# Performance work log

Measured on AMD Instinct MI355X. Metric: run time of the kernel, lower is better.

## Reference

```python
import jax, jax.numpy as jnp
import numpy as np

VOCAB, E, H, L, B, T, S, V = 32000, 512, 1024, 2, 64, 64, 128, 1024
LSTM_IN = 2 * E  # input_feed=True -> cat(embed, prev_output)


def setup_inputs() -> dict:
    key = jax.random.key(0)
    ks = jax.random.split(key, 12)
    s = lambda *d: 1.0 / np.sqrt(d[-1])
    return {
        "tgt_batch": jax.random.randint(ks[0], (T, B), 0, VOCAB),
        "h_encoder": jax.random.normal(ks[1], (B, S, V), jnp.float32),
        "emb": jax.random.normal(ks[2], (VOCAB, E), jnp.float32) * 0.02,
        "output_init": jnp.zeros((B, E), jnp.float32),
        "hidden_init": jnp.zeros((L, B, H), jnp.float32),
        "W_ih": jax.random.uniform(ks[3], (L, 4 * H, LSTM_IN), jnp.float32, -s(H), s(H)),
        "W_hh": jax.random.uniform(ks[4], (L, 4 * H, H), jnp.float32, -s(H), s(H)),
        "b_ih": jax.random.uniform(ks[5], (L, 4 * H), jnp.float32, -s(H), s(H)),
        "b_hh": jax.random.uniform(ks[6], (L, 4 * H), jnp.float32, -s(H), s(H)),
        "W1": jax.random.uniform(ks[7], (V, H), jnp.float32, -s(H), s(H)),   # query_size->values_size
        "b1": jnp.zeros((V,), jnp.float32),
        "W2": jax.random.uniform(ks[8], (E, H + V), jnp.float32, -s(H + V), s(H + V)),
        "b2": jnp.zeros((E,), jnp.float32),
    }


def reference(tgt_batch, h_encoder, emb, output_init, hidden_init,
              W_ih, W_hh, b_ih, b_hh, W1, b1, W2, b2):
    x_seq = emb[tgt_batch]  # [T, B, E]

    def lstm_cell(x, h, c):  # x:[B,2E], h/c:[L,B,H]
        hs, cs, inp = [], [], x
        for l in range(L):
            gates = inp @ W_ih[l].T + b_ih[l] + h[l] @ W_hh[l].T + b_hh[l]
            i, f, g, o = jnp.split(gates, 4, axis=-1)  # torch gate order i,f,g,o
            c_new = jax.nn.sigmoid(f) * c[l] + jax.nn.sigmoid(i) * jnp.tanh(g)
            h_new = jax.nn.sigmoid(o) * jnp.tanh(c_new)
            hs.append(h_new); cs.append(c_new); inp = h_new
        return jnp.stack(hs), jnp.stack(cs), inp

    def global_attn(query):  # query:[B,H]
        q = query @ W1.T + b1                              # [B,V]
        scores = jnp.einsum('bv,bsv->bs', q, h_encoder)    # [B,S]
        a = jax.nn.softmax(scores, axis=-1)
        attended = jnp.einsum('bs,bsv->bv', a, h_encoder)  # [B,V]
        return jnp.tanh(jnp.concatenate([attended, query], axis=-1) @ W2.T + b2)

    def step(carry, x):
        h, c, out = carry
        inp = jnp.concatenate([x, out], axis=-1)  # input feed
        h, c, top = lstm_cell(inp, h, c)
        o = global_attn(top)  # dropout is identity in eval mode
        return (h, c, o), o

    c0 = jnp.zeros_like(hidden_init)
    _, outs = jax.lax.scan(step, (hidden_init, c0, output_init), x_seq)
    return jnp.transpose(outs, (1, 0, 2))  # [B, T, E]
```

## Files before the change

kernel.cpp:

```cpp
#include <hip/hip_runtime.h>

typedef _Float16 f16;
typedef f16 f16x8 __attribute__((ext_vector_type(8)));
typedef f16 f16x2 __attribute__((ext_vector_type(2)));
typedef float f32x4 __attribute__((ext_vector_type(4)));
typedef unsigned long long u64;

#define MFMA16(a, b, c) __builtin_amdgcn_mfma_f32_16x16x32_f16(a, b, c, 0, 0, 0)
#define ROT 16

__device__ inline float fsig(float x) { return 1.f / (1.f + __expf(-x)); }
__device__ inline float ftanh(float x) {
    x = fminf(15.f, fmaxf(-15.f, x));
    float e = __expf(2.f * x);
    return (e - 1.f) / (e + 1.f);
}

__device__ __forceinline__ void bstore8(void* p, u64 v) {
    __hip_atomic_store((u64*)p, v, __ATOMIC_RELAXED, __HIP_MEMORY_SCOPE_AGENT);
}
__device__ __forceinline__ void bstore4(float* p, float v) {
    __hip_atomic_store(p, v, __ATOMIC_RELAXED, __HIP_MEMORY_SCOPE_AGENT);
}
__device__ __forceinline__ float bload_f32(const float* p) {
    return __hip_atomic_load((float*)p, __ATOMIC_RELAXED, __HIP_MEMORY_SCOPE_AGENT);
}
__device__ __forceinline__ void fstore_u32(unsigned* p, unsigned v) {
    __hip_atomic_store(p, v, __ATOMIC_RELAXED, __HIP_MEMORY_SCOPE_AGENT);
}
__device__ __forceinline__ unsigned fload_u32(unsigned* p) {
    return __hip_atomic_load(p, __ATOMIC_RELAXED, __HIP_MEMORY_SCOPE_AGENT);
}

__device__ __forceinline__ void poll4(unsigned* f, unsigned e, int lane) {
    for (;;) {
        unsigned v = fload_u32(f + (lane & 3));
        if (__all((int)(v >= e))) break;
        __builtin_amdgcn_s_sleep(1);
    }
    asm volatile("" ::: "memory");
}

__global__ __launch_bounds__(256) void k_convert(
    const float* __restrict__ Wih, const float* __restrict__ Whh,
    const float* __restrict__ W1, const float* __restrict__ W2,
    const float* __restrict__ bih, const float* __restrict__ bhh,
    const int* __restrict__ tgt, const float* __restrict__ emb,
    const float* __restrict__ henc,
    f16* __restrict__ wcat, f16* __restrict__ w1c, f16* __restrict__ w2a,
    f16* __restrict__ w2b, float* __restrict__ bsum, f16* __restrict__ Xall,
    f16* __restrict__ h16)
{
    const long NW = 16777216, NT = 1048576, NA = 524288, NB = 524288,
               NS = 8192, NX = 2097152, NH = 8388608;
    const long TOT = NW + NT + NA + NB + NS + NX + NH;
    for (long i = (long)blockIdx.x * 256 + threadIdx.x; i < TOT;
         i += (long)gridDim.x * 256) {
        if (i < NW) {
            long l = i >> 23;
            long r = i & 8388607;
            int j = (int)(r >> 11), k = (int)(r & 2047);
            float val = (k < 1024) ? Wih[(l * 4096 + j) * 1024 + k]
                                   : Whh[(l * 4096 + j) * 1024 + (k - 1024)];
            wcat[i] = (f16)val;
        } else if (i < NW + NT) {
            long r = i - NW;
            int h = (int)(r >> 10), v = (int)(r & 1023);
            w1c[r] = (f16)W1[(long)v * 1024 + h];
        } else if (i < NW + NT + NA) {
            long r = i - NW - NT;
            int e = (int)(r >> 10), v = (int)(r & 1023);
            w2a[r] = (f16)W2[(long)e * 2048 + v];
        } else if (i < NW + NT + NA + NB) {
            long r = i - NW - NT - NA;
            int e = (int)(r >> 10), k = (int)(r & 1023);
            w2b[r] = (f16)W2[(long)e * 2048 + 1024 + k];
        } else if (i < NW + NT + NA + NB + NS) {
            long r = i - NW - NT - NA - NB;
            bsum[r] = bih[r] + bhh[r];
        } else if (i < NW + NT + NA + NB + NS + NX) {
            long r = i - NW - NT - NA - NB - NS;
            int t = (int)(r >> 15), mm = (int)((r >> 9) & 63), k = (int)(r & 511);
            Xall[r] = (f16)emb[(long)tgt[t * 64 + mm] * 512 + k];
        } else {
            long r = i - NW - NT - NA - NB - NS - NX;
            h16[r] = (f16)henc[r];
        }
    }
}

__global__ __launch_bounds__(256) void k_init(
    const float* __restrict__ oinit, const float* __restrict__ hinit,
    f16* __restrict__ O0, f16* __restrict__ H00, f16* __restrict__ H10,
    float* __restrict__ c01, unsigned* __restrict__ sync)
{
    int idx = blockIdx.x * 256 + threadIdx.x;
    if (idx < 32768) {
        O0[idx] = (f16)oinit[idx];
    } else if (idx < 98304) {
        H00[idx - 32768] = (f16)hinit[idx - 32768];
    } else if (idx < 163840) {
        H10[idx - 98304] = (f16)hinit[65536 + (idx - 98304)];
    } else if (idx < 294912) {
        c01[idx - 163840] = 0.f;
    } else if (idx < 297984) {
        sync[idx - 294912] = 0u;
    }
}

__global__ __launch_bounds__(256) void k_sb(
    const float* __restrict__ b1, const float* __restrict__ henc,
    float* __restrict__ sb)
{
    int bs = blockIdx.x * 256 + threadIdx.x;
    const float* hr = henc + (long)bs * 1024;
    float a = 0.f;
    for (int k = 0; k < 1024; k += 4) {
        float4 h4 = *(const float4*)(hr + k);
        float4 b4 = *(const float4*)(b1 + k);
        a += h4.x * b4.x + h4.y * b4.y + h4.z * b4.z + h4.w * b4.w;
    }
    sb[bs] = a;
}

__global__ __launch_bounds__(256) void k_gemm(
    const f16* __restrict__ A, const f16* __restrict__ Bm,
    f16* __restrict__ C, int N)
{
    int nb = N >> 7;
    int bm = blockIdx.x / nb, bn = blockIdx.x % nb;
    int tid = threadIdx.x, w = tid >> 6, lane = tid & 63;
    int quad = lane >> 4, nn = lane & 15;
    const f16* ap = A + (long)(bm * 64 + w * 16 + nn) * 1024 + quad * 8;
    const f16* bp = Bm + (long)(bn * 128 + nn) * 1024 + quad * 8;
    f32x4 acc[8] = {};
    for (int kk = 0; kk < 1024; kk += 32) {
        f16x8 av = *(const f16x8*)(ap + kk);
        #pragma unroll
        for (int t2 = 0; t2 < 8; ++t2) {
            f16x8 bv = *(const f16x8*)(bp + (long)t2 * 16 * 1024 + kk);
            acc[t2] = MFMA16(av, bv, acc[t2]);
        }
    }
    #pragma unroll
    for (int t2 = 0; t2 < 8; ++t2)
        #pragma unroll
        for (int r = 0; r < 4; ++r) {
            int m = bm * 64 + w * 16 + quad * 4 + r;
            int col = bn * 128 + t2 * 16 + nn;
            C[(long)m * N + col] = (f16)acc[t2][r];
        }
}

__device__ __forceinline__ void gsync(unsigned* sync, unsigned e) {
    asm volatile("s_waitcnt vmcnt(0) lgkmcnt(0)" ::: "memory");
    __syncthreads();
    unsigned* arr = sync;
    unsigned* rel = sync + 256;
    if (threadIdx.x == 0)
        fstore_u32(arr + blockIdx.x, e);
    if (blockIdx.x == 0) {
        if (threadIdx.x < 64) {
            int lane = threadIdx.x;
            for (;;) {
                unsigned v0 = fload_u32(arr + lane);
                unsigned v1 = fload_u32(arr + 64 + lane);
                unsigned v2 = fload_u32(arr + 128 + lane);
                unsigned v3 = fload_u32(arr + 192 + lane);
                if (__all((int)(v0 >= e && v1 >= e && v2 >= e && v3 >= e)))
                    break;
                __builtin_amdgcn_s_sleep(1);
            }
            if (lane < 8) fstore_u32(rel + lane * 32, e);
        }
    } else if (threadIdx.x == 0) {
        unsigned* r = rel + (blockIdx.x & 7) * 32;
        while (fload_u32(r) < e)
            __builtin_amdgcn_s_sleep(2);
    }
    __syncthreads();
    asm volatile("" ::: "memory");
}

__device__ __forceinline__ void lstm_core(
    const f16* base, int rst, const f16x8* wreg,
    const float* __restrict__ bs_, float* __restrict__ c_,
    f16* __restrict__ dest, float* lds, int b, int tid)
{
    int w = tid >> 6, lane = tid & 63, quad = lane >> 4, n = lane & 15;
    const f16* ap = base + (long)n * rst + quad * 8;
    f32x4 acc0 = {}, acc1 = {}, acc2 = {}, acc3 = {};
    #pragma unroll
    for (int kk = 0; kk < 8; ++kk) {
        f16x8 bv = wreg[kk];
        f16x8 a0 = *(const f16x8*)(ap + kk * 32);
        f16x8 a1 = *(const f16x8*)(ap + (long)16 * rst + kk * 32);
        f16x8 a2 = *(const f16x8*)(ap + (long)32 * rst + kk * 32);
        f16x8 a3 = *(const f16x8*)(ap + (long)48 * rst + kk * 32);
        acc0 = MFMA16(a0, bv, acc0);
        acc1 = MFMA16(a1, bv, acc1);
        acc2 = MFMA16(a2, bv, acc2);
        acc3 = MFMA16(a3, bv, acc3);
    }
    #pragma unroll
    for (int r = 0; r < 4; ++r) {
        int mb = quad * 4 + r;
        lds[(w * 64 + mb) * 17 + n]      = acc0[r];
        lds[(w * 64 + 16 + mb) * 17 + n] = acc1[r];
        lds[(w * 64 + 32 + mb) * 17 + n] = acc2[r];
        lds[(w * 64 + 48 + mb) * 17 + n] = acc3[r];
    }
    __syncthreads();
    if (tid < 256) {
        int m = tid >> 2, uu = tid & 3;
        float s0 = 0.f, s1 = 0.f, s2 = 0.f, s3 = 0.f;
        #pragma unroll
        for (int ww = 0; ww < 8; ++ww) {
            const float* p = lds + (ww * 64 + m) * 17 + uu * 4;
            s0 += p[0]; s1 += p[1]; s2 += p[2]; s3 += p[3];
        }
        int ug = b * 4 + uu;
        float iv = fsig(s0 + bs_[ug]);
        float fv = fsig(s1 + bs_[1024 + ug]);
        float gv = ftanh(s2 + bs_[2048 + ug]);
        float ov = fsig(s3 + bs_[3072 + ug]);
        float cold = c_[m * 1024 + ug];
        float cn = fv * cold + iv * gv;
        float hn = ov * ftanh(cn);
        c_[m * 1024 + ug] = cn;
        lds[8704 + m * 4 + uu] = hn;
    }
    __syncthreads();
    if (tid < 64) {
        union { f16 h[4]; u64 u; } pk;
        #pragma unroll
        for (int uu = 0; uu < 4; ++uu) pk.h[uu] = (f16)lds[8704 + tid * 4 + uu];
        bstore8(dest + (long)tid * 1024 + b * 4, pk.u);
    }
}

__global__ __launch_bounds__(512, 2) void k_persist(
    const f16* __restrict__ wcat, const float* __restrict__ bsum,
    float* __restrict__ c01, const f16* __restrict__ Xall,
    f16* __restrict__ Orot, f16* __restrict__ H0rot, f16* __restrict__ H1rot,
    const f16* __restrict__ P16, const f16* __restrict__ Q216,
    const f16* __restrict__ w2b, const float* __restrict__ sb,
    const float* __restrict__ b2, float* __restrict__ out,
    float* __restrict__ Z2p, float* __restrict__ Z2s,
    unsigned* __restrict__ sync)
{
    extern __shared__ float smem[];
    float* scr = smem;
    f16* h1l = (f16*)(smem + 8960);
    f16* Pl  = (f16*)(smem + 9472);
    f16* Q2l = Pl + 32768;

    int b = blockIdx.x, tid = threadIdx.x;
    int m = b >> 2, sq = b & 3;
    int wv = tid >> 6, lane = tid & 63, quad = lane >> 4, nn = lane & 15;
    unsigned* ggf = sync + 1024;

    f16x8 w0[8], w1[8];
    {
        int j0 = (nn & 3) * 1024 + b * 4 + (nn >> 2);
        const f16* wp = wcat + (long)j0 * 2048 + wv * 256 + quad * 8;
        #pragma unroll
        for (int kk = 0; kk < 8; ++kk) {
            w0[kk] = *(const f16x8*)(wp + kk * 32);
            w1[kk] = *(const f16x8*)(wp + 8388608 + kk * 32);
        }
    }
    {
        const uint4* gp = (const uint4*)(P16 + ((long)(m * 128 + sq * 32)) * 1024);
        #pragma unroll
        for (int i = 0; i < 8; ++i) ((uint4*)Pl)[i * 512 + tid] = gp[i * 512 + tid];
        const uint4* gq = (const uint4*)(Q216 + ((long)(m * 128 + sq * 32)) * 512);
        #pragma unroll
        for (int i = 0; i < 4; ++i) ((uint4*)Q2l)[i * 512 + tid] = gq[i * 512 + tid];
    }
    __syncthreads();

    unsigned epoch = 0;
    for (int t = 0; t < 64; ++t) {
        int rs0 = t & (ROT - 1), rs1 = (t + 1) & (ROT - 1);
        const f16* Xc = Xall + (long)t * 32768;
        const f16* Oc = Orot + (long)rs0 * 32768;
        const f16* H0c = H0rot + (long)rs0 * 65536;
        f16* H0n = H0rot + (long)rs1 * 65536;
        const f16* H1c = H1rot + (long)rs0 * 65536;
        f16* H1n = H1rot + (long)rs1 * 65536;

        {
            const f16* base; int rst;
            if (wv < 2)      { base = Xc + wv * 256;        rst = 512; }
            else if (wv < 4) { base = Oc + (wv - 2) * 256;  rst = 512; }
            else             { base = H0c + (wv - 4) * 256; rst = 1024; }
            lstm_core(base, rst, w0, bsum, c01, H0n, scr, b, tid);
        }
        gsync(sync, ++epoch);

        {
            const f16* base = (wv < 4) ? (H0n + wv * 256) : (H1c + (wv - 4) * 256);
            lstm_core(base, 1024, w1, bsum + 4096, c01 + 65536, H1n, scr, b, tid);
        }
        gsync(sync, ++epoch);

        {
            if (tid < 128)
                ((uint4*)h1l)[tid] = *(const uint4*)(H1n + (long)m * 1024 + tid * 8);
            __syncthreads();

            {
                int el = tid >> 2, kq = tid & 3;
                int eg = sq * 128 + el;
                const f16* wp2 = w2b + (long)eg * 1024 + kq * 256;
                const f16* hp = h1l + kq * 256;
                float z1 = 0.f;
                #pragma unroll 8
                for (int i = 0; i < 32; ++i) {
                    f16x8 wv8 = *(const f16x8*)(wp2 + i * 8);
                    f16x8 hv8 = *(const f16x8*)(hp + i * 8);
                    #pragma unroll
                    for (int p2 = 0; p2 < 4; ++p2) {
                        f16x2 wa = { wv8[p2 * 2], wv8[p2 * 2 + 1] };
                        f16x2 ha = { hv8[p2 * 2], hv8[p2 * 2 + 1] };
                        z1 = __builtin_amdgcn_fdot2(wa, ha, z1, false);
                    }
                }
                z1 += __shfl_xor(z1, 1);
                z1 += __shfl_xor(z1, 2);
                if (kq == 0) scr[8736 + el] = z1 + b2[eg];
            }

            int sl = tid >> 4, kc = tid & 15;
            const f16* prow = Pl + sl * 1024;
            float a0 = 0.f;
            #pragma unroll
            for (int i = 0; i < 8; ++i) {
                int ch = (i * 16 + kc) * 8;
                f16x8 pv = *(const f16x8*)(prow + ch);
                f16x8 hv = *(const f16x8*)(h1l + ch);
                #pragma unroll
                for (int p2 = 0; p2 < 4; ++p2) {
                    f16x2 pa = { pv[p2 * 2], pv[p2 * 2 + 1] };
                    f16x2 ha = { hv[p2 * 2], hv[p2 * 2 + 1] };
                    a0 = __builtin_amdgcn_fdot2(pa, ha, a0, false);
                }
            }
            #pragma unroll
            for (int off = 8; off; off >>= 1) a0 += __shfl_xor(a0, off, 16);
            if (kc == 0)
                scr[8704 + sl] = a0 + sb[m * 128 + sq * 32 + sl];
            __syncthreads();

            if (tid < 32) {
                float v = scr[8704 + tid];
                float mx = v;
                #pragma unroll
                for (int off = 16; off; off >>= 1) mx = fmaxf(mx, __shfl_xor(mx, off));
                float ev = __expf(v - mx);
                float sm = ev;
                #pragma unroll
                for (int off = 16; off; off >>= 1) sm += __shfl_xor(sm, off);
                scr[8704 + tid] = ev;
                if (tid == 0) {
                    union { float f[2]; u64 u; } pk;
                    pk.f[0] = mx; pk.f[1] = sm;
                    bstore8(Z2s + ((m * 4 + sq) << 1), pk.u);
                }
            }
            __syncthreads();

            float zp = 0.f;
            #pragma unroll 8
            for (int jy = 0; jy < 32; ++jy)
                zp += scr[8704 + jy] * (float)Q2l[jy * 512 + tid];
            bstore4(Z2p + ((m * 4 + sq) << 9) + tid, zp);

            asm volatile("s_waitcnt vmcnt(0)" ::: "memory");
            __syncthreads();
            if (tid == 0) fstore_u32(ggf + m * 32 + sq, (unsigned)(t + 1));
            if (tid < 64) poll4(ggf + m * 32, (unsigned)(t + 1), tid);
            __syncthreads();

            if (tid < 8) scr[8864 + tid] = bload_f32(Z2s + m * 8 + tid);
            __syncthreads();
            if (tid < 128) {
                float m0 = scr[8864], s0q = scr[8865], m1 = scr[8866], s1q = scr[8867],
                      m2 = scr[8868], s2q = scr[8869], m3 = scr[8870], s3q = scr[8871];
                float M = fmaxf(fmaxf(m0, m1), fmaxf(m2, m3));
                float q0 = __expf(m0 - M), q1 = __expf(m1 - M),
                      q2 = __expf(m2 - M), q3 = __expf(m3 - M);
                float den = q0 * s0q + q1 * s1q + q2 * s2q + q3 * s3q;
                int e2 = sq * 128 + tid;
                float num = q0 * bload_f32(Z2p + ((m * 4 + 0) << 9) + e2)
                          + q1 * bload_f32(Z2p + ((m * 4 + 1) << 9) + e2)
                          + q2 * bload_f32(Z2p + ((m * 4 + 2) << 9) + e2)
                          + q3 * bload_f32(Z2p + ((m * 4 + 3) << 9) + e2);
                float z = scr[8736 + tid] + num / den;
                float o = ftanh(z);
                out[((long)m * 64 + t) * 512 + e2] = o;
                ((f16*)(scr + 8880))[tid] = (f16)o;
            }
            __syncthreads();
            if (tid < 32) {
                f16* ob = (f16*)(scr + 8880);
                union { f16 h[4]; u64 u; } pk;
                #pragma unroll
                for (int i = 0; i < 4; ++i) pk.h[i] = ob[tid * 4 + i];
                bstore8(Orot + (long)rs1 * 32768 + m * 512 + sq * 128 + tid * 4, pk.u);
            }
        }
        gsync(sync, ++epoch);
    }
}

extern "C" void kernel_launch(void* const* d_in, const int* in_sizes, int n_in,
                              void* d_out, int out_size, void* d_ws, size_t ws_size,
                              hipStream_t stream)
{
    const int*   tgt   = (const int*)d_in[0];
    const float* henc  = (const float*)d_in[1];
    const float* emb   = (const float*)d_in[2];
    const float* oinit = (const float*)d_in[3];
    const float* hinit = (const float*)d_in[4];
    const float* Wih   = (const float*)d_in[5];
    const float* Whh   = (const float*)d_in[6];
    const float* bih   = (const float*)d_in[7];
    const float* bhh   = (const float*)d_in[8];
    const float* W1    = (const float*)d_in[9];
    const float* b1    = (const float*)d_in[10];
    const float* W2    = (const float*)d_in[11];
    const float* b2    = (const float*)d_in[12];
    float* out = (float*)d_out;

    char* ws = (char*)d_ws;
    f16*      wcat  = (f16*)(ws + 0);
    f16*      P16   = (f16*)(ws + 33554432);
    f16*      Q216  = (f16*)(ws + 50331648);
    f16*      h16   = (f16*)(ws + 58720256);
    f16*      w2b   = (f16*)(ws + 75497472);
    f16*      w1c   = (f16*)(ws + 76546048);
    f16*      w2a   = (f16*)(ws + 78643200);
    f16*      Xall  = (f16*)(ws + 79691776);
    f16*      H0rot = (f16*)(ws + 83886080);
    f16*      H1rot = (f16*)(ws + 85983232);
    f16*      Orot  = (f16*)(ws + 88080384);
    float*    c01   = (float*)(ws + 89128960);
    float*    Z2p   = (float*)(ws + 58720256);
    float*    Z2s   = (float*)(ws + 90439680);
    float*    bsum  = (float*)(ws + 90472448);
    float*    sb    = (float*)(ws + 90505216);
    unsigned* sync  = (unsigned*)(ws + 90537984);

    hipLaunchKernelGGL(k_convert, dim3(4096), dim3(256), 0, stream,
                       Wih, Whh, W1, W2, bih, bhh, tgt, emb, henc,
                       wcat, w1c, w2a, w2b, bsum, Xall, h16);
    hipLaunchKernelGGL(k_init, dim3(1164), dim3(256), 0, stream,
                       oinit, hinit, Orot, H0rot, H1rot, c01, sync);
    hipLaunchKernelGGL(k_sb, dim3(32), dim3(256), 0, stream, b1, henc, sb);
    hipLaunchKernelGGL(k_gemm, dim3(128 * 8), dim3(256), 0, stream,
                       h16, w1c, P16, 1024);
    hipLaunchKernelGGL(k_gemm, dim3(128 * 4), dim3(256), 0, stream,
                       h16, w2a, Q216, 512);

    static const unsigned LDS_BYTES = 9472 * 4 + 32768 * 2 + 16384 * 2;
    hipFuncSetAttribute((const void*)k_persist,
                        hipFuncAttributeMaxDynamicSharedMemorySize, LDS_BYTES);
    void* args[] = { &wcat, &bsum, &c01, &Xall, &Orot, &H0rot, &H1rot, &P16,
                     &Q216, &w2b, &sb, &b2, &out, &Z2p, &Z2s, &sync };
    hipLaunchCooperativeKernel((const void*)k_persist, dim3(256), dim3(512),
                               args, LDS_BYTES, stream);
}
```

Measured before the change: 2.549 ms.

## Split W2b projection across four blocks per row with transposed weights

The query part of the output projection (W2b·h1) is now split by K across the four blocks that share a batch row, instead of each block computing its 128 outputs over the full K. Each block computes 512 partial sums over 256 K values with coalesced reads from a transposed W2b, writes them to a global scratch, and the final stage sums the four partials. This cuts the per-block serial dot length and improves coalescing. In exchange it adds global traffic and relies on the existing grid sync for visibility. The inner loop is also now scalar fp32 with strided loads instead of fdot2.

Result: faster. 2.436 ms (-4.4%).

```diff
diff --git a/kernel.cpp b/kernel.cpp
--- a/kernel.cpp
+++ b/kernel.cpp
@@ -48,7 +48,7 @@
     const int* __restrict__ tgt, const float* __restrict__ emb,
     const float* __restrict__ henc,
     f16* __restrict__ wcat, f16* __restrict__ w1c, f16* __restrict__ w2a,
-    f16* __restrict__ w2b, float* __restrict__ bsum, f16* __restrict__ Xall,
+    f16* __restrict__ w2bT, float* __restrict__ bsum, f16* __restrict__ Xall,
     f16* __restrict__ h16)
 {
     const long NW = 16777216, NT = 1048576, NA = 524288, NB = 524288,
@@ -73,8 +73,8 @@
             w2a[r] = (f16)W2[(long)e * 2048 + v];
         } else if (i < NW + NT + NA + NB) {
             long r = i - NW - NT - NA;
-            int e = (int)(r >> 10), k = (int)(r & 1023);
-            w2b[r] = (f16)W2[(long)e * 2048 + 1024 + k];
+            int k = (int)(r >> 9), e = (int)(r & 511);
+            w2bT[r] = (f16)W2[(long)e * 2048 + 1024 + k];
         } else if (i < NW + NT + NA + NB + NS) {
             long r = i - NW - NT - NA - NB;
             bsum[r] = bih[r] + bhh[r];
@@ -244,10 +244,10 @@
     float* __restrict__ c01, const f16* __restrict__ Xall,
     f16* __restrict__ Orot, f16* __restrict__ H0rot, f16* __restrict__ H1rot,
     const f16* __restrict__ P16, const f16* __restrict__ Q216,
-    const f16* __restrict__ w2b, const float* __restrict__ sb,
+    const f16* __restrict__ w2bT, const float* __restrict__ sb,
     const float* __restrict__ b2, float* __restrict__ out,
-    float* __restrict__ Z2p, float* __restrict__ Z2s,
-    unsigned* __restrict__ sync)
+    float* __restrict__ Z1p, float* __restrict__ Z2p,
+    float* __restrict__ Z2s, unsigned* __restrict__ sync)
 {
     extern __shared__ float smem[];
     float* scr = smem;
@@ -311,25 +311,14 @@
             __syncthreads();
 
             {
-                int el = tid >> 2, kq = tid & 3;
-                int eg = sq * 128 + el;
-                const f16* wp2 = w2b + (long)eg * 1024 + kq * 256;
-                const f16* hp = h1l + kq * 256;
+                const f16* wt = w2bT + ((long)(sq * 256) << 9) + tid;
+                const f16* hp = h1l + sq * 256;
                 float z1 = 0.f;
                 #pragma unroll 8
-                for (int i = 0; i < 32; ++i) {
-                    f16x8 wv8 = *(const f16x8*)(wp2 + i * 8);
-                    f16x8 hv8 = *(const f16x8*)(hp + i * 8);
-                    #pragma unroll
-                    for (int p2 = 0; p2 < 4; ++p2) {
-                        f16x2 wa = { wv8[p2 * 2], wv8[p2 * 2 + 1] };
-                        f16x2 ha = { hv8[p2 * 2], hv8[p2 * 2 + 1] };
-                        z1 = __builtin_amdgcn_fdot2(wa, ha, z1, false);
-                    }
-                }
-                z1 += __shfl_xor(z1, 1);
-                z1 += __shfl_xor(z1, 2);
-                if (kq == 0) scr[8736 + el] = z1 + b2[eg];
+                for (int k = 0; k < 256; ++k)
+                    z1 += (float)hp[k] * (float)wt[(long)k << 9];
+                if (sq == 0) z1 += b2[tid];
+                bstore4(Z1p + ((m * 4 + sq) << 9) + tid, z1);
             }
 
             int sl = tid >> 4, kc = tid & 15;
@@ -393,11 +382,15 @@
                       q2 = __expf(m2 - M), q3 = __expf(m3 - M);
                 float den = q0 * s0q + q1 * s1q + q2 * s2q + q3 * s3q;
                 int e2 = sq * 128 + tid;
+                float z = bload_f32(Z1p + ((m * 4 + 0) << 9) + e2)
+                        + bload_f32(Z1p + ((m * 4 + 1) << 9) + e2)
+                        + bload_f32(Z1p + ((m * 4 + 2) << 9) + e2)
+                        + bload_f32(Z1p + ((m * 4 + 3) << 9) + e2);
                 float num = q0 * bload_f32(Z2p + ((m * 4 + 0) << 9) + e2)
                           + q1 * bload_f32(Z2p + ((m * 4 + 1) << 9) + e2)
                           + q2 * bload_f32(Z2p + ((m * 4 + 2) << 9) + e2)
                           + q3 * bload_f32(Z2p + ((m * 4 + 3) << 9) + e2);
-                float z = scr[8736 + tid] + num / den;
+                z += num / den;
                 float o = ftanh(z);
                 out[((long)m * 64 + t) * 512 + e2] = o;
                 ((f16*)(scr + 8880))[tid] = (f16)o;
@@ -439,7 +432,7 @@
     f16*      P16   = (f16*)(ws + 33554432);
     f16*      Q216  = (f16*)(ws + 50331648);
     f16*      h16   = (f16*)(ws + 58720256);
-    f16*      w2b   = (f16*)(ws + 75497472);
+    f16*      w2bT  = (f16*)(ws + 75497472);
     f16*      w1c   = (f16*)(ws + 76546048);
     f16*      w2a   = (f16*)(ws + 78643200);
     f16*      Xall  = (f16*)(ws + 79691776);
@@ -447,7 +440,8 @@
     f16*      H1rot = (f16*)(ws + 85983232);
     f16*      Orot  = (f16*)(ws + 88080384);
     float*    c01   = (float*)(ws + 89128960);
-    float*    Z2p   = (float*)(ws + 58720256);
+    float*    Z1p   = (float*)(ws + 58720256);
+    float*    Z2p   = (float*)(ws + 59244544);
     float*    Z2s   = (float*)(ws + 90439680);
     float*    bsum  = (float*)(ws + 90472448);
     float*    sb    = (float*)(ws + 90505216);
@@ -455,7 +449,7 @@
 
     hipLaunchKernelGGL(k_convert, dim3(4096), dim3(256), 0, stream,
                        Wih, Whh, W1, W2, bih, bhh, tgt, emb, henc,
-                       wcat, w1c, w2a, w2b, bsum, Xall, h16);
+                       wcat, w1c, w2a, w2bT, bsum, Xall, h16);
     hipLaunchKernelGGL(k_init, dim3(1164), dim3(256), 0, stream,
                        oinit, hinit, Orot, H0rot, H1rot, c01, sync);
     hipLaunchKernelGGL(k_sb, dim3(32), dim3(256), 0, stream, b1, henc, sb);
@@ -468,7 +462,7 @@
     hipFuncSetAttribute((const void*)k_persist,
                         hipFuncAttributeMaxDynamicSharedMemorySize, LDS_BYTES);
     void* args[] = { &wcat, &bsum, &c01, &Xall, &Orot, &H0rot, &H1rot, &P16,
-                     &Q216, &w2b, &sb, &b2, &out, &Z2p, &Z2s, &sync };
+                     &Q216, &w2bT, &sb, &b2, &out, &Z1p, &Z2p, &Z2s, &sync };
     hipLaunchCooperativeKernel((const void*)k_persist, dim3(256), dim3(512),
                                args, LDS_BYTES, stream);
 }
```
